# Performance work log

Hardware: AMD Instinct MI355X
Metric: run time of the kernel (lower is better)

The kernel has to match this reference:

```python
import jax, jax.numpy as jnp
import numpy as np

N = 100_000
E = 1_600_000
IN_DIM = 3
HID = 64
NUM_CLASSES = 3
BN_EPS = 1e-5


def setup_inputs() -> dict:
    key = jax.random.key(0)
    ks = jax.random.split(key, 16)
    x = jax.random.normal(ks[0], (N, IN_DIM), dtype=jnp.float32)
    row = jax.random.randint(ks[1], (E,), 0, N, dtype=jnp.int32)
    col = jax.random.randint(ks[2], (E,), 0, N, dtype=jnp.int32)
    vals = jax.random.uniform(ks[3], (E,), dtype=jnp.float32)
    # parameters
    W1 = jax.random.normal(ks[4], (IN_DIM, HID), dtype=jnp.float32) / np.sqrt(IN_DIM)
    b1 = jnp.zeros((HID,), jnp.float32)
    W2 = jax.random.normal(ks[5], (HID, HID), dtype=jnp.float32) / np.sqrt(HID)
    b2 = jnp.zeros((HID,), jnp.float32)
    g1 = jnp.ones((HID,), jnp.float32)
    be1 = jnp.zeros((HID,), jnp.float32)
    m1 = jax.random.normal(ks[6], (HID,), dtype=jnp.float32) * 0.1
    v1 = jax.random.uniform(ks[7], (HID,), dtype=jnp.float32) + 0.5
    g2 = jnp.ones((HID,), jnp.float32)
    be2 = jnp.zeros((HID,), jnp.float32)
    m2 = jax.random.normal(ks[8], (HID,), dtype=jnp.float32) * 0.1
    v2 = jax.random.uniform(ks[9], (HID,), dtype=jnp.float32) + 0.5
    Wc = jax.random.normal(ks[10], (2 * HID, NUM_CLASSES), dtype=jnp.float32) / np.sqrt(2 * HID)
    bc = jnp.zeros((NUM_CLASSES,), jnp.float32)
    return dict(x=x, row=row, col=col, vals=vals, W1=W1, b1=b1, g1=g1, be1=be1,
                m1=m1, v1=v1, W2=W2, b2=b2, g2=g2, be2=be2, m2=m2, v2=v2,
                Wc=Wc, bc=bc)


def _spmm(row, col, vals, h):
    # sparse [N,N] @ dense [N,H] via gather + segment_sum
    return jax.ops.segment_sum(vals[:, None] * h[col], row, num_segments=N)


def _bn_eval(h, g, be, m, v):
    return (h - m) * jax.lax.rsqrt(v + BN_EPS) * g + be


def reference(x, row, col, vals, W1, b1, g1, be1, m1, v1,
              W2, b2, g2, be2, m2, v2, Wc, bc):
    h = _spmm(row, col, vals, x @ W1 + b1)          # [N, HID]
    h = jax.nn.relu(_bn_eval(h, g1, be1, m1, v1))   # eval: dropout no-op
    h = _spmm(row, col, vals, h @ W2 + b2)          # [N, HID]
    h = jax.nn.relu(_bn_eval(h, g2, be2, m2, v2))
    g = jnp.concatenate([h.mean(axis=0), h.max(axis=0)], axis=0)  # [2*HID]
    return g @ Wc + bc                               # [NUM_CLASSES]
```

## Files before the change

### kernel.cpp

```cpp
#include <hip/hip_runtime.h>
#include <hip/hip_bf16.h>

#define HID 64
#define BN_EPS 1e-5f
#define BROWS 256
#define MAXB 512
#define BCAP 4608
#define BATCH 4096
#define S2STRIDE 4096

typedef __attribute__((ext_vector_type(8))) short bf16x8;
typedef __attribute__((ext_vector_type(4))) float f32x4;

__global__ __launch_bounds__(512) void zero_bcur_k(int* __restrict__ bcur) {
  bcur[threadIdx.x] = 0;
}

__global__ __launch_bounds__(256) void bucketA_k(
    const int* __restrict__ row, const int* __restrict__ col,
    const float* __restrict__ vals, int* __restrict__ bcur,
    int2* __restrict__ bucketed, int E, int NB) {
  __shared__ int cnt[MAXB];
  __shared__ int scn[MAXB];
  __shared__ int cnt2[MAXB];
  __shared__ int gbase[MAXB];
  __shared__ int2 stg[BATCH];
  __shared__ unsigned short stgb[BATCH];
  int t = threadIdx.x;
  int start = blockIdx.x * BATCH;
  for (int i = t; i < MAXB; i += 256) cnt[i] = 0;
  __syncthreads();
#pragma unroll
  for (int k = 0; k < BATCH / 256; ++k) {
    int i = start + k * 256 + t;
    if (i < E) atomicAdd(&cnt[row[i] >> 8], 1);
  }
  __syncthreads();
  int i0 = t, i1 = t + 256;
  scn[i0] = cnt[i0]; scn[i1] = cnt[i1];
  __syncthreads();
  for (int off = 1; off < 512; off <<= 1) {
    int a0 = (i0 >= off) ? scn[i0 - off] : 0;
    int a1 = (i1 >= off) ? scn[i1 - off] : 0;
    __syncthreads();
    scn[i0] += a0; scn[i1] += a1;
    __syncthreads();
  }
  cnt2[i0] = scn[i0] - cnt[i0];
  cnt2[i1] = scn[i1] - cnt[i1];
  for (int b = t; b < NB; b += 256)
    if (cnt[b] > 0) gbase[b] = atomicAdd(&bcur[b], cnt[b]);
  __syncthreads();
#pragma unroll
  for (int k = 0; k < BATCH / 256; ++k) {
    int i = start + k * 256 + t;
    if (i < E) {
      int r = row[i];
      int b = r >> 8;
      int pos = atomicAdd(&cnt2[b], 1);
      stg[pos] = make_int2(((r & 255) << 17) | col[i], __float_as_int(vals[i]));
      stgb[pos] = (unsigned short)b;
    }
  }
  __syncthreads();
  int m = min(BATCH, E - start);
  for (int s = t; s < m; s += 256) {
    int b = stgb[s];
    int lbase = scn[b] - cnt[b];
    bucketed[(size_t)b * BCAP + gbase[b] + (s - lbase)] = stg[s];
  }
}

__global__ __launch_bounds__(256) void bucketB_k(
    const int2* __restrict__ bucketed, const int* __restrict__ bcnt,
    const float* __restrict__ x,
    const float* __restrict__ W1, const float* __restrict__ b1,
    const float* __restrict__ g, const float* __restrict__ be,
    const float* __restrict__ m, const float* __restrict__ v,
    const float* __restrict__ W2, const float* __restrict__ b2,
    int2* __restrict__ cv, int* __restrict__ rowstart, int* __restrict__ rowend,
    __hip_bfloat16* __restrict__ out, int N) {
  __shared__ int rcnt[BROWS];
  __shared__ int scn[BROWS];
  __shared__ int rcur[BROWS];
  __shared__ float axs[BROWS][4];
  int b = blockIdx.x;
  int t = threadIdx.x;
  int lane = t & 63;
  int wv = t >> 6;
  int li = lane & 15;
  int lk = lane >> 4;
  float A0[16], A1[16], A2[16], A3[16], SS[16];
#pragma unroll
  for (int s = 0; s < 2; ++s)
#pragma unroll
    for (int j = 0; j < 8; ++j) {
      int f = 32 * s + 8 * lk + j;
      float scale = g[f] * rsqrtf(v[f] + BN_EPS);
      float shift = fmaf(-m[f], scale, be[f]);
      int idx = s * 8 + j;
      A0[idx] = scale * W1[0 * HID + f];
      A1[idx] = scale * W1[1 * HID + f];
      A2[idx] = scale * W1[2 * HID + f];
      A3[idx] = scale * b1[f];
      SS[idx] = shift;
    }
  bf16x8 bfr[4][2];
#pragma unroll
  for (int c = 0; c < 4; ++c)
#pragma unroll
    for (int s = 0; s < 2; ++s)
#pragma unroll
      for (int j = 0; j < 8; ++j) {
        int k = 32 * s + 8 * lk + j;
        __hip_bfloat16 hb = __float2bfloat16(W2[k * HID + 16 * c + li]);
        bfr[c][s][j] = *reinterpret_cast<short*>(&hb);
      }
  float b2c[4];
#pragma unroll
  for (int c = 0; c < 4; ++c) b2c[c] = b2[16 * c + li];

  size_t rbase = (size_t)b * BCAP;
  int cnt = bcnt[b];
  int rows = min(BROWS, N - b * BROWS);
  rcnt[t] = 0;
  __syncthreads();
  for (int i = t; i < cnt; i += 256) {
    int2 e = bucketed[rbase + i];
    atomicAdd(&rcnt[e.x >> 17], 1);
  }
  __syncthreads();
  scn[t] = rcnt[t];
  __syncthreads();
  for (int off = 1; off < 256; off <<= 1) {
    int vv = (t >= off) ? scn[t - off] : 0;
    __syncthreads();
    scn[t] += vv;
    __syncthreads();
  }
  int excl = scn[t] - rcnt[t];
  rcur[t] = excl;
  if (t < rows) {
    rowstart[b * BROWS + t] = (int)rbase + excl;
    rowend[b * BROWS + t] = (int)rbase + excl + rcnt[t];
  }
  __syncthreads();
  for (int i = t; i < cnt; i += 256) {
    int2 e = bucketed[rbase + i];
    int pos = atomicAdd(&rcur[e.x >> 17], 1);
    cv[rbase + pos] = make_int2(e.x & 0x1FFFF, e.y);
  }
  __syncthreads();
  int grp = t >> 4, L = t & 15;
  for (int pass = 0; pass < 16; ++pass) {
    int lrow = pass * 16 + grp;
    int s0 = scn[lrow] - rcnt[lrow];
    int e0 = scn[lrow];
    float a0 = 0.f, a1 = 0.f, a2 = 0.f, a3 = 0.f;
    for (int i2 = s0 + L; i2 < e0; i2 += 16) {
      int2 eg = cv[rbase + i2];
      const float* xp = x + 3 * (size_t)eg.x;
      float vv = __int_as_float(eg.y);
      a0 = fmaf(vv, xp[0], a0);
      a1 = fmaf(vv, xp[1], a1);
      a2 = fmaf(vv, xp[2], a2);
      a3 += vv;
    }
#pragma unroll
    for (int msk = 8; msk >= 1; msk >>= 1) {
      a0 += __shfl_xor(a0, msk, 64);
      a1 += __shfl_xor(a1, msk, 64);
      a2 += __shfl_xor(a2, msk, 64);
      a3 += __shfl_xor(a3, msk, 64);
    }
    if (L == 0) {
      axs[lrow][0] = a0; axs[lrow][1] = a1;
      axs[lrow][2] = a2; axs[lrow][3] = a3;
    }
  }
  __syncthreads();
  for (int it = 0; it < 4; ++it) {
    int rb = wv * 4 + it;
    int lrow = rb * 16 + li;
    float a0 = axs[lrow][0], a1 = axs[lrow][1],
          a2 = axs[lrow][2], a3 = axs[lrow][3];
    bf16x8 afr[2];
#pragma unroll
    for (int s = 0; s < 2; ++s)
#pragma unroll
      for (int j = 0; j < 8; ++j) {
        int idx = s * 8 + j;
        float z = fmaf(a0, A0[idx],
                  fmaf(a1, A1[idx],
                  fmaf(a2, A2[idx],
                  fmaf(a3, A3[idx], SS[idx]))));
        float u = fmaxf(z, 0.f);
        __hip_bfloat16 hb = __float2bfloat16(u);
        afr[s][j] = *reinterpret_cast<short*>(&hb);
      }
    f32x4 acc0 = {0.f, 0.f, 0.f, 0.f}, acc1 = {0.f, 0.f, 0.f, 0.f};
    f32x4 acc2 = {0.f, 0.f, 0.f, 0.f}, acc3 = {0.f, 0.f, 0.f, 0.f};
    acc0 = __builtin_amdgcn_mfma_f32_16x16x32_bf16(afr[0], bfr[0][0], acc0, 0, 0, 0);
    acc0 = __builtin_amdgcn_mfma_f32_16x16x32_bf16(afr[1], bfr[0][1], acc0, 0, 0, 0);
    acc1 = __builtin_amdgcn_mfma_f32_16x16x32_bf16(afr[0], bfr[1][0], acc1, 0, 0, 0);
    acc1 = __builtin_amdgcn_mfma_f32_16x16x32_bf16(afr[1], bfr[1][1], acc1, 0, 0, 0);
    acc2 = __builtin_amdgcn_mfma_f32_16x16x32_bf16(afr[0], bfr[2][0], acc2, 0, 0, 0);
    acc2 = __builtin_amdgcn_mfma_f32_16x16x32_bf16(afr[1], bfr[2][1], acc2, 0, 0, 0);
    acc3 = __builtin_amdgcn_mfma_f32_16x16x32_bf16(afr[0], bfr[3][0], acc3, 0, 0, 0);
    acc3 = __builtin_amdgcn_mfma_f32_16x16x32_bf16(afr[1], bfr[3][1], acc3, 0, 0, 0);
#pragma unroll
    for (int r = 0; r < 4; ++r) {
      int orow = b * BROWS + rb * 16 + 4 * lk + r;
      if (orow < N) {
        size_t ob = (size_t)orow * HID + li;
        out[ob + 0]  = __float2bfloat16(acc0[r] + b2c[0]);
        out[ob + 16] = __float2bfloat16(acc1[r] + b2c[1]);
        out[ob + 32] = __float2bfloat16(acc2[r] + b2c[2]);
        out[ob + 48] = __float2bfloat16(acc3[r] + b2c[3]);
      }
    }
  }
}

__global__ __launch_bounds__(256) void spmm2_pool_k(
    const int* __restrict__ rowstart, const int* __restrict__ rowend,
    const int2* __restrict__ cv,
    const __hip_bfloat16* __restrict__ hb,
    const float* __restrict__ g, const float* __restrict__ be,
    const float* __restrict__ m, const float* __restrict__ v,
    float* __restrict__ pS, float* __restrict__ pM, int N) {
  int lane = threadIdx.x & 63;
  int wid = threadIdx.x >> 6;
  int grp = lane >> 3;
  int gl = lane & 7;
  int base = grp << 3;
  float scl[8], shf[8];
#pragma unroll
  for (int j = 0; j < 8; ++j) {
    int f = gl * 8 + j;
    float sc = g[f] * rsqrtf(v[f] + BN_EPS);
    scl[j] = sc;
    shf[j] = fmaf(-m[f], sc, be[f]);
  }
  const uint4* __restrict__ h4 = (const uint4*)hb;
  float psum[8] = {0.f,0.f,0.f,0.f,0.f,0.f,0.f,0.f};
  float pmax[8] = {0.f,0.f,0.f,0.f,0.f,0.f,0.f,0.f};
  int rowstep = gridDim.x * 32;
  for (int r = blockIdx.x * 32 + wid * 8 + grp; r < N; r += rowstep) {
    int s = rowstart[r], e = rowend[r];
    float acc[8] = {0.f,0.f,0.f,0.f,0.f,0.f,0.f,0.f};
    for (int i = s; i < e; i += 8) {
      int take = e - i; if (take > 8) take = 8;
      int2 my = cv[i + (gl < take ? gl : take - 1)];
      int cj[8]; float vj[8];
#pragma unroll
      for (int j = 0; j < 8; ++j) {
        cj[j] = __shfl(my.x, base + j, 64);
        float vv = __uint_as_float((uint)__shfl(my.y, base + j, 64));
        vj[j] = (j < take) ? vv : 0.f;
      }
      uint4 hv[8];
#pragma unroll
      for (int j = 0; j < 8; ++j) hv[j] = h4[(size_t)cj[j] * 8 + gl];
#pragma unroll
      for (int j = 0; j < 8; ++j) {
        acc[0] = fmaf(vj[j], __uint_as_float(hv[j].x << 16), acc[0]);
        acc[1] = fmaf(vj[j], __uint_as_float(hv[j].x & 0xffff0000u), acc[1]);
        acc[2] = fmaf(vj[j], __uint_as_float(hv[j].y << 16), acc[2]);
        acc[3] = fmaf(vj[j], __uint_as_float(hv[j].y & 0xffff0000u), acc[3]);
        acc[4] = fmaf(vj[j], __uint_as_float(hv[j].z << 16), acc[4]);
        acc[5] = fmaf(vj[j], __uint_as_float(hv[j].z & 0xffff0000u), acc[5]);
        acc[6] = fmaf(vj[j], __uint_as_float(hv[j].w << 16), acc[6]);
        acc[7] = fmaf(vj[j], __uint_as_float(hv[j].w & 0xffff0000u), acc[7]);
      }
    }
#pragma unroll
    for (int j = 0; j < 8; ++j) {
      float hvl = fmaxf(fmaf(acc[j], scl[j], shf[j]), 0.f);
      psum[j] += hvl;
      pmax[j] = fmaxf(pmax[j], hvl);
    }
  }
  __shared__ float ls[32][HID], lm[32][HID];
  int slot = wid * 8 + grp;
#pragma unroll
  for (int j = 0; j < 8; ++j) {
    ls[slot][gl * 8 + j] = psum[j];
    lm[slot][gl * 8 + j] = pmax[j];
  }
  __syncthreads();
  int t = threadIdx.x;
  if (t < HID) {
    float s32 = 0.f, m32 = 0.f;
#pragma unroll
    for (int kk = 0; kk < 32; ++kk) {
      s32 += ls[kk][t];
      m32 = fmaxf(m32, lm[kk][t]);
    }
    pS[(size_t)t * S2STRIDE + blockIdx.x] = s32;
    pM[(size_t)t * S2STRIDE + blockIdx.x] = m32;
  }
}

__global__ __launch_bounds__(256) void pool_reduce_k(
    const float* __restrict__ pS, const float* __restrict__ pM,
    float* __restrict__ gsum, float* __restrict__ gmaxf, int nblk) {
  int f = blockIdx.x;
  int t = threadIdx.x;
  float s = 0.f, m = 0.f;
  for (int j = t; j < nblk; j += 256) {
    s += pS[(size_t)f * S2STRIDE + j];
    m = fmaxf(m, pM[(size_t)f * S2STRIDE + j]);
  }
#pragma unroll
  for (int msk = 32; msk >= 1; msk >>= 1) {
    s += __shfl_xor(s, msk, 64);
    m = fmaxf(m, __shfl_xor(m, msk, 64));
  }
  __shared__ float ws_[4], wm_[4];
  if ((t & 63) == 0) { ws_[t >> 6] = s; wm_[t >> 6] = m; }
  __syncthreads();
  if (t == 0) {
    s = ws_[0] + ws_[1] + ws_[2] + ws_[3];
    m = fmaxf(fmaxf(wm_[0], wm_[1]), fmaxf(wm_[2], wm_[3]));
    gsum[f] = s;
    gmaxf[f] = m;
  }
}

__global__ __launch_bounds__(128) void final_k(
    const float* __restrict__ gsum, const float* __restrict__ gmaxf,
    const float* __restrict__ Wc, const float* __restrict__ bc,
    float* __restrict__ out, float invN) {
  __shared__ float red[128 * 3];
  int j = threadIdx.x;
  float gj = (j < HID) ? gsum[j] * invN : gmaxf[j - HID];
#pragma unroll
  for (int c = 0; c < 3; ++c) red[j * 3 + c] = gj * Wc[j * 3 + c];
  __syncthreads();
  for (int off = 64; off >= 1; off >>= 1) {
    if (j < off) {
#pragma unroll
      for (int c = 0; c < 3; ++c) red[j * 3 + c] += red[(j + off) * 3 + c];
    }
    __syncthreads();
  }
  if (j < 3) out[j] = red[j] + bc[j];
}

extern "C" void kernel_launch(void* const* d_in, const int* in_sizes, int n_in,
                              void* d_out, int out_size, void* d_ws, size_t ws_size,
                              hipStream_t stream) {
  const float* x    = (const float*)d_in[0];
  const int*   row  = (const int*)d_in[1];
  const int*   col  = (const int*)d_in[2];
  const float* vals = (const float*)d_in[3];
  const float* W1   = (const float*)d_in[4];
  const float* b1   = (const float*)d_in[5];
  const float* g1   = (const float*)d_in[6];
  const float* be1  = (const float*)d_in[7];
  const float* m1   = (const float*)d_in[8];
  const float* v1   = (const float*)d_in[9];
  const float* W2   = (const float*)d_in[10];
  const float* b2   = (const float*)d_in[11];
  const float* g2   = (const float*)d_in[12];
  const float* be2  = (const float*)d_in[13];
  const float* m2   = (const float*)d_in[14];
  const float* v2   = (const float*)d_in[15];
  const float* Wc   = (const float*)d_in[16];
  const float* bc   = (const float*)d_in[17];
  float* out = (float*)d_out;

  const int N = in_sizes[0] / 3;
  const int E = in_sizes[1];
  const int NB = (N + BROWS - 1) / BROWS;
  const int S2G = (N + 31) / 32;

  __hip_bfloat16* wsA = (__hip_bfloat16*)d_ws;
  int2* bucketed = (int2*)(wsA + (size_t)N * HID);
  int2* cv = bucketed + (size_t)MAXB * BCAP;
  int* rowstart = (int*)(cv + (size_t)MAXB * BCAP);
  int* rowend = rowstart + N;
  int* bcur = rowend + N;
  float* pS = (float*)(bcur + MAXB);
  float* pM = pS + (size_t)HID * S2STRIDE;
  float* gsum = pM + (size_t)HID * S2STRIDE;
  float* gmaxf = gsum + HID;

  zero_bcur_k<<<1, 512, 0, stream>>>(bcur);
  bucketA_k<<<(E + BATCH - 1) / BATCH, 256, 0, stream>>>(row, col, vals, bcur, bucketed, E, NB);
  bucketB_k<<<NB, 256, 0, stream>>>(bucketed, bcur, x,
                                    W1, b1, g1, be1, m1, v1, W2, b2,
                                    cv, rowstart, rowend, wsA, N);

  spmm2_pool_k<<<S2G, 256, 0, stream>>>(rowstart, rowend, cv, wsA, g2, be2, m2, v2, pS, pM, N);
  pool_reduce_k<<<HID, 256, 0, stream>>>(pS, pM, gsum, gmaxf, S2G);
  final_k<<<1, 128, 0, stream>>>(gsum, gmaxf, Wc, bc, out, 1.0f / (float)N);
}
```

Before: 117.4 us.

## Stage bucket edges in LDS and fuse first-layer aggregation into scatter pass

Each bucket's edges are now staged in shared memory on the first read, so the second pass reads from LDS instead of global memory. The layer-1 aggregation of x is folded into the scatter loop using shared-memory float atomics, which removes the separate per-row gather pass, its shuffle reduction and a barrier. The cost is 36 KB of extra LDS per block, which may lower occupancy, plus atomic contention on per-row accumulators. Float atomics also make the summation order nondeterministic.

Measured after the change: 133.1 us. 13.4% more time.

```diff
diff --git a/kernel.cpp b/kernel.cpp
--- a/kernel.cpp
+++ b/kernel.cpp
@@ -84,6 +84,7 @@
   __shared__ int scn[BROWS];
   __shared__ int rcur[BROWS];
   __shared__ float axs[BROWS][4];
+  __shared__ int2 stg[BCAP];
   int b = blockIdx.x;
   int t = threadIdx.x;
   int lane = t & 63;
@@ -124,9 +125,12 @@
   int cnt = bcnt[b];
   int rows = min(BROWS, N - b * BROWS);
   rcnt[t] = 0;
+#pragma unroll
+  for (int k = 0; k < 4; ++k) axs[t][k] = 0.f;
   __syncthreads();
   for (int i = t; i < cnt; i += 256) {
     int2 e = bucketed[rbase + i];
+    stg[i] = e;
     atomicAdd(&rcnt[e.x >> 17], 1);
   }
   __syncthreads();
@@ -146,37 +150,17 @@
   }
   __syncthreads();
   for (int i = t; i < cnt; i += 256) {
-    int2 e = bucketed[rbase + i];
-    int pos = atomicAdd(&rcur[e.x >> 17], 1);
-    cv[rbase + pos] = make_int2(e.x & 0x1FFFF, e.y);
-  }
-  __syncthreads();
-  int grp = t >> 4, L = t & 15;
-  for (int pass = 0; pass < 16; ++pass) {
-    int lrow = pass * 16 + grp;
-    int s0 = scn[lrow] - rcnt[lrow];
-    int e0 = scn[lrow];
-    float a0 = 0.f, a1 = 0.f, a2 = 0.f, a3 = 0.f;
-    for (int i2 = s0 + L; i2 < e0; i2 += 16) {
-      int2 eg = cv[rbase + i2];
-      const float* xp = x + 3 * (size_t)eg.x;
-      float vv = __int_as_float(eg.y);
-      a0 = fmaf(vv, xp[0], a0);
-      a1 = fmaf(vv, xp[1], a1);
-      a2 = fmaf(vv, xp[2], a2);
-      a3 += vv;
-    }
-#pragma unroll
-    for (int msk = 8; msk >= 1; msk >>= 1) {
-      a0 += __shfl_xor(a0, msk, 64);
-      a1 += __shfl_xor(a1, msk, 64);
-      a2 += __shfl_xor(a2, msk, 64);
-      a3 += __shfl_xor(a3, msk, 64);
-    }
-    if (L == 0) {
-      axs[lrow][0] = a0; axs[lrow][1] = a1;
-      axs[lrow][2] = a2; axs[lrow][3] = a3;
-    }
+    int2 e = stg[i];
+    int lr = e.x >> 17;
+    int c = e.x & 0x1FFFF;
+    int pos = atomicAdd(&rcur[lr], 1);
+    cv[rbase + pos] = make_int2(c, e.y);
+    float vv = __int_as_float(e.y);
+    const float* xp = x + 3 * (size_t)c;
+    atomicAdd(&axs[lr][0], vv * xp[0]);
+    atomicAdd(&axs[lr][1], vv * xp[1]);
+    atomicAdd(&axs[lr][2], vv * xp[2]);
+    atomicAdd(&axs[lr][3], vv);
   }
   __syncthreads();
   for (int it = 0; it < 4; ++it) {
```
